# Kernel optimization log

Measured on AMD Instinct MI355X. Metric: run time of the kernel, lower is better.

## Reference

```python
import jax, jax.numpy as jnp
import numpy as np

N_NODES = 50000
N_EDGES = 300000
D = 256
N_RELS = 500


def setup_inputs() -> dict:
    key = jax.random.key(0)
    ks = jax.random.split(key, 12)
    s = 1.0 / np.sqrt(D)  # keep activations O(1) through the dense transforms
    return {
        "h": jax.random.normal(ks[0], (N_NODES, D), dtype=jnp.float32),
        "prev_h": jax.random.normal(ks[1], (N_NODES, D), dtype=jnp.float32),
        "emb_rel": jax.random.normal(ks[2], (N_RELS, D), dtype=jnp.float32),
        "norm": jax.random.uniform(ks[3], (N_NODES, 1), dtype=jnp.float32),
        "weight_neighbor": jax.random.normal(ks[4], (D, D), dtype=jnp.float32) * s,
        "loop_weight": jax.random.normal(ks[5], (D, D), dtype=jnp.float32) * s,
        "evolve_loop_weight": jax.random.normal(ks[6], (D, D), dtype=jnp.float32) * s,
        "skip_connect_weight": jax.random.normal(ks[7], (D, D), dtype=jnp.float32) * s,
        "skip_connect_bias": jnp.zeros((D,), dtype=jnp.float32),
        "src": jax.random.randint(ks[8], (N_EDGES,), 0, N_NODES),
        "dst": jax.random.randint(ks[9], (N_EDGES,), 0, N_NODES),
        "etype": jax.random.randint(ks[10], (N_EDGES,), 0, N_RELS),
    }


def reference(h, prev_h, emb_rel, norm, weight_neighbor, loop_weight,
              evolve_loop_weight, skip_connect_weight, skip_connect_bias,
              src, dst, etype):
    n_nodes = h.shape[0]
    # msg_func: per-edge gather of src features + relation embedding, dense transform
    msg = (h[src] + emb_rel[etype]) @ weight_neighbor          # [E, D]
    # fn.sum: segment-sum messages into destination nodes
    agg = jax.ops.segment_sum(msg, dst, num_segments=n_nodes)  # [N, D]
    # apply_func: multiply by per-node norm
    agg = agg * norm
    # self-loop: loop_weight where in_degree > 0, evolve_loop_weight otherwise
    in_deg = jax.ops.segment_sum(jnp.ones_like(dst), dst, num_segments=n_nodes)
    has_in = (in_deg > 0)[:, None]
    loop_message = jnp.where(has_in, h @ loop_weight, h @ evolve_loop_weight)
    # skip connection gate
    skip_weight = jax.nn.sigmoid(prev_h @ skip_connect_weight + skip_connect_bias)
    node_repr = skip_weight * (agg + loop_message) + (1.0 - skip_weight) * prev_h
    return jax.nn.relu(node_repr)
```

## Files before the change

### kernel.cpp

```cpp
#include <hip/hip_runtime.h>
#include <cstdint>
#include <cstddef>

#define N_NODES 50000
#define N_EDGES 300000
#define DIM     256
#define KTOT    768
#define N_RELS  500

#define SCAN_BLK  256
#define SCAN_NBLK ((N_NODES + SCAN_BLK - 1) / SCAN_BLK)

typedef unsigned short u16;
typedef __attribute__((ext_vector_type(8))) short short8v;
typedef __attribute__((ext_vector_type(4))) float float4v;

static __device__ __forceinline__ u16 f2bf(float f) {
    union { float f; unsigned u; } v; v.f = f;
    unsigned u = v.u;
    unsigned r = u + 0x7FFFu + ((u >> 16) & 1u);
    return (u16)(r >> 16);
}
static __device__ __forceinline__ float bf2f(u16 b) {
    union { unsigned u; float f; } v; v.u = ((unsigned)b) << 16; return v.f;
}

static __device__ __forceinline__ void gld16(const void* g, u16* l) {
    __builtin_amdgcn_global_load_lds(
        (const __attribute__((address_space(1))) unsigned int*)g,
        (__attribute__((address_space(3))) unsigned int*)l,
        16, 0, 0);
}

__global__ void conv_kernel(const float* __restrict__ h, const float* __restrict__ emb,
                            u16* __restrict__ Xcat, u16* __restrict__ embb) {
    int i = blockIdx.x * blockDim.x + threadIdx.x;
    int e0 = i * 8;
    if (e0 >= (N_NODES + N_RELS) * DIM) return;
    const float* src; u16* dst;
    if (e0 < N_NODES * DIM) {
        int n = e0 >> 8, c = e0 & 255;
        src = h + e0;
        dst = Xcat + (size_t)n * 512 + 256 + c;
    } else {
        int off = e0 - N_NODES * DIM;
        src = emb + off; dst = embb + off;
    }
    float4 a = *(const float4*)(src);
    float4 b = *(const float4*)(src + 4);
    u16 o[8] = { f2bf(a.x), f2bf(a.y), f2bf(a.z), f2bf(a.w),
                 f2bf(b.x), f2bf(b.y), f2bf(b.z), f2bf(b.w) };
    *(uint4*)dst = *(const uint4*)o;
}

__global__ void wt_kernel(const float* __restrict__ Wn, const float* __restrict__ Wl,
                          const float* __restrict__ Wsc, u16* __restrict__ Wt) {
    int k = blockIdx.x;
    int d = threadIdx.x;
    const float* W = (k < 256) ? Wn : ((k < 512) ? Wl : Wsc);
    int kk = k & 255;
    Wt[(size_t)d * KTOT + k] = f2bf(W[kk * DIM + d]);
}

__global__ void hist_kernel(const int* __restrict__ dstv, int* __restrict__ deg) {
    int e = blockIdx.x * 256 + threadIdx.x;
    if (e < N_EDGES) atomicAdd(&deg[dstv[e]], 1);
}

__global__ void scanA_kernel(const int* __restrict__ deg, int* __restrict__ excl_local,
                             int* __restrict__ block_sum) {
    __shared__ int sdata[SCAN_BLK];
    int t = threadIdx.x, i = blockIdx.x * SCAN_BLK + t;
    int v = (i < N_NODES) ? deg[i] : 0;
    sdata[t] = v;
    __syncthreads();
    for (int off = 1; off < SCAN_BLK; off <<= 1) {
        int u = (t >= off) ? sdata[t - off] : 0;
        __syncthreads();
        sdata[t] += u;
        __syncthreads();
    }
    if (i < N_NODES) excl_local[i] = sdata[t] - v;
    if (t == SCAN_BLK - 1) block_sum[blockIdx.x] = sdata[t];
}

__global__ void scanB_kernel(const int* __restrict__ block_sum, int* __restrict__ block_base,
                             int* __restrict__ offsets) {
    __shared__ int sdata[SCAN_NBLK];
    int t = threadIdx.x;
    int v = (t < SCAN_NBLK) ? block_sum[t] : 0;
    if (t < SCAN_NBLK) sdata[t] = v;
    __syncthreads();
    for (int off = 1; off < SCAN_NBLK; off <<= 1) {
        int u = (t >= off && t < SCAN_NBLK) ? sdata[t - off] : 0;
        __syncthreads();
        if (t < SCAN_NBLK) sdata[t] += u;
        __syncthreads();
    }
    if (t < SCAN_NBLK) block_base[t] = sdata[t] - v;
    if (t == SCAN_NBLK - 1) offsets[N_NODES] = sdata[t];
}

__global__ void scanC_kernel(const int* __restrict__ excl_local, const int* __restrict__ block_base,
                             int* __restrict__ offsets, int* __restrict__ cursor) {
    int i = blockIdx.x * SCAN_BLK + threadIdx.x;
    if (i < N_NODES) {
        int e = block_base[blockIdx.x] + excl_local[i];
        offsets[i] = e; cursor[i] = e;
    }
}

__global__ void scatter_kernel(const int* __restrict__ src, const int* __restrict__ dstv,
                               const int* __restrict__ et, int* __restrict__ cursor,
                               unsigned* __restrict__ esee) {
    int e = blockIdx.x * 256 + threadIdx.x;
    if (e >= N_EDGES) return;
    int d = dstv[e];
    int pos = atomicAdd(&cursor[d], 1);
    esee[pos] = (unsigned)src[e] * N_RELS + (unsigned)et[e];
}

__global__ void agg_kernel(u16* __restrict__ Xcat, const u16* __restrict__ embb,
                           const float* __restrict__ norm, const int* __restrict__ offsets,
                           const unsigned* __restrict__ esee,
                           int* __restrict__ wl_count, int* __restrict__ wl) {
    int wave = (blockIdx.x * 256 + threadIdx.x) >> 6;
    int lane = threadIdx.x & 63;
    if (wave >= N_NODES) return;
    int n = wave;
    int s0 = offsets[n], s1 = offsets[n + 1];
    int c4 = lane * 4;
    float4 acc = make_float4(0.f, 0.f, 0.f, 0.f);
    int e = s0;
    for (; e + 1 < s1; e += 2) {
        unsigned v0 = esee[e], v1 = esee[e + 1];
        unsigned sa = v0 / N_RELS, ta = v0 - sa * N_RELS;
        unsigned sb = v1 / N_RELS, tb = v1 - sb * N_RELS;
        ushort4 ha = *(const ushort4*)(Xcat + (size_t)sa * 512 + 256 + c4);
        ushort4 ea = *(const ushort4*)(embb + (size_t)ta * DIM + c4);
        ushort4 hb = *(const ushort4*)(Xcat + (size_t)sb * 512 + 256 + c4);
        ushort4 eb = *(const ushort4*)(embb + (size_t)tb * DIM + c4);
        acc.x += bf2f(ha.x) + bf2f(ea.x) + bf2f(hb.x) + bf2f(eb.x);
        acc.y += bf2f(ha.y) + bf2f(ea.y) + bf2f(hb.y) + bf2f(eb.y);
        acc.z += bf2f(ha.z) + bf2f(ea.z) + bf2f(hb.z) + bf2f(eb.z);
        acc.w += bf2f(ha.w) + bf2f(ea.w) + bf2f(hb.w) + bf2f(eb.w);
    }
    if (e < s1) {
        unsigned v = esee[e];
        unsigned s = v / N_RELS;
        unsigned t = v - s * N_RELS;
        ushort4 hv = *(const ushort4*)(Xcat + (size_t)s * 512 + 256 + c4);
        ushort4 ev = *(const ushort4*)(embb + (size_t)t * DIM + c4);
        acc.x += bf2f(hv.x) + bf2f(ev.x);
        acc.y += bf2f(hv.y) + bf2f(ev.y);
        acc.z += bf2f(hv.z) + bf2f(ev.z);
        acc.w += bf2f(hv.w) + bf2f(ev.w);
    }
    float nr = norm[n];
    u16 o[4] = { f2bf(acc.x * nr), f2bf(acc.y * nr), f2bf(acc.z * nr), f2bf(acc.w * nr) };
    *(ushort4*)(Xcat + (size_t)n * 512 + c4) = *(const ushort4*)o;
    if (lane == 0 && s1 == s0) { int idx = atomicAdd(wl_count, 1); wl[idx] = n; }
}

__launch_bounds__(256, 2)
__global__ void gemm_kernel(const u16* __restrict__ Xcat, const u16* __restrict__ Wt,
                            const float* __restrict__ prev_h, const float* __restrict__ bias,
                            float* __restrict__ out) {
    __shared__ __align__(16) u16 lds[40960];
    int tid  = threadIdx.x;
    int wave = tid >> 6, lane = tid & 63, q = lane >> 4, m16 = lane & 15;
    int wn = wave * 64;
    int m0 = blockIdx.x * 64;
    int lr = lane >> 3, lc8 = lane & 7;
    int scol = (lc8 ^ lr) << 3;

    int ar0 = wave * 16 + lr, ar1 = ar0 + 8;
    int ga0 = (m0 + ar0 < N_NODES) ? (m0 + ar0) : (N_NODES - 1);
    int ga1 = (m0 + ar1 < N_NODES) ? (m0 + ar1) : (N_NODES - 1);
    const u16*   sA0 = Xcat   + (size_t)ga0 * 512 + scol;
    const u16*   sA1 = Xcat   + (size_t)ga1 * 512 + scol;
    const float* pP0 = prev_h + (size_t)ga0 * 256 + scol;
    const float* pP1 = prev_h + (size_t)ga1 * 256 + scol;
    const u16*   sB  = Wt + (size_t)(wave * 64 + lr) * KTOT + scol;
    int ldsA_w = wave * 16 * 64;
    int ldsB_w = 8192 + wave * 64 * 64;

    float4v acc1[4][4], acc2[4][4];
#pragma unroll
    for (int i = 0; i < 4; i++)
#pragma unroll
        for (int j = 0; j < 4; j++) { acc1[i][j] = (float4v)0.f; acc2[i][j] = (float4v)0.f; }

#pragma unroll
    for (int j = 0; j < 8; j++)
        gld16(sB + (size_t)j * 8 * KTOT, &lds[ldsB_w + j * 512]);
    gld16(sA0, &lds[ldsA_w]);
    gld16(sA1, &lds[ldsA_w + 512]);
    __syncthreads();

    int sw = (m16 & 7) << 3;

#pragma unroll
    for (int kt = 0; kt < 12; kt++) {
        int buf = kt & 1, nbuf = buf ^ 1;
        float pf0[8], pf1[8];
        if (kt < 11) {
            int kn = kt + 1;
#pragma unroll
            for (int j = 0; j < 8; j++)
                gld16(sB + (size_t)j * 8 * KTOT + kn * 64,
                      &lds[ldsB_w + nbuf * 16384 + j * 512]);
            if (kn < 8) {
                gld16(sA0 + kn * 64, &lds[ldsA_w + nbuf * 4096]);
                gld16(sA1 + kn * 64, &lds[ldsA_w + nbuf * 4096 + 512]);
            } else {
                const float* p0 = pP0 + (kn - 8) * 64;
                const float* p1 = pP1 + (kn - 8) * 64;
                float4 x0 = *(const float4*)p0, y0 = *(const float4*)(p0 + 4);
                float4 x1 = *(const float4*)p1, y1 = *(const float4*)(p1 + 4);
                pf0[0] = x0.x; pf0[1] = x0.y; pf0[2] = x0.z; pf0[3] = x0.w;
                pf0[4] = y0.x; pf0[5] = y0.y; pf0[6] = y0.z; pf0[7] = y0.w;
                pf1[0] = x1.x; pf1[1] = x1.y; pf1[2] = x1.z; pf1[3] = x1.w;
                pf1[4] = y1.x; pf1[5] = y1.y; pf1[6] = y1.z; pf1[7] = y1.w;
            }
        }
#pragma unroll
        for (int kk = 0; kk < 2; kk++) {
            int ck = (kk * 32 + q * 8) ^ sw;
            short8v af[4], bfr[4];
#pragma unroll
            for (int mi = 0; mi < 4; mi++)
                af[mi] = *(const short8v*)(&lds[buf * 4096 + (mi * 16 + m16) * 64 + ck]);
#pragma unroll
            for (int ni = 0; ni < 4; ni++)
                bfr[ni] = *(const short8v*)(&lds[8192 + buf * 16384 + (wn + ni * 16 + m16) * 64 + ck]);
            if (kt < 8) {
#pragma unroll
                for (int mi = 0; mi < 4; mi++)
#pragma unroll
                    for (int ni = 0; ni < 4; ni++)
                        acc1[mi][ni] = __builtin_amdgcn_mfma_f32_16x16x32_bf16(
                            af[mi], bfr[ni], acc1[mi][ni], 0, 0, 0);
            } else {
#pragma unroll
                for (int mi = 0; mi < 4; mi++)
#pragma unroll
                    for (int ni = 0; ni < 4; ni++)
                        acc2[mi][ni] = __builtin_amdgcn_mfma_f32_16x16x32_bf16(
                            af[mi], bfr[ni], acc2[mi][ni], 0, 0, 0);
            }
        }
        if (kt < 11 && kt + 1 >= 8) {
            u16 o0[8] = { f2bf(pf0[0]), f2bf(pf0[1]), f2bf(pf0[2]), f2bf(pf0[3]),
                          f2bf(pf0[4]), f2bf(pf0[5]), f2bf(pf0[6]), f2bf(pf0[7]) };
            u16 o1[8] = { f2bf(pf1[0]), f2bf(pf1[1]), f2bf(pf1[2]), f2bf(pf1[3]),
                          f2bf(pf1[4]), f2bf(pf1[5]), f2bf(pf1[6]), f2bf(pf1[7]) };
            *(uint4*)(&lds[nbuf * 4096 + ar0 * 64 + lc8 * 8]) = *(const uint4*)o0;
            *(uint4*)(&lds[nbuf * 4096 + ar1 * 64 + lc8 * 8]) = *(const uint4*)o1;
        }
        __syncthreads();
    }

#pragma unroll
    for (int mi = 0; mi < 4; mi++) {
#pragma unroll
        for (int ni = 0; ni < 4; ni++) {
            int d = wn + ni * 16 + m16;
            float b = bias[d];
#pragma unroll
            for (int r = 0; r < 4; r++) {
                int node = m0 + mi * 16 + q * 4 + r;
                if (node < N_NODES) {
                    float S  = acc2[mi][ni][r] + b;
                    float sg = 1.f / (1.f + __expf(-S));
                    float ph = prev_h[(size_t)node * DIM + d];
                    float v  = sg * acc1[mi][ni][r] + (1.f - sg) * ph;
                    out[(size_t)node * DIM + d] = fmaxf(v, 0.f);
                }
            }
        }
    }
}

__global__ void fixup_kernel(const float* __restrict__ h, const float* __restrict__ prev_h,
                             const float* __restrict__ We, const float* __restrict__ Wsc,
                             const float* __restrict__ bias, const int* __restrict__ wl_count,
                             const int* __restrict__ wl, float* __restrict__ out) {
    __shared__ float ph[DIM], hh[DIM];
    int d = threadIdx.x;
    int cnt = *wl_count;
    for (int i = blockIdx.x; i < cnt; i += gridDim.x) {
        int n = wl[i];
        ph[d] = prev_h[(size_t)n * DIM + d];
        hh[d] = h[(size_t)n * DIM + d];
        __syncthreads();
        float s = 0.f, l = 0.f;
        for (int k = 0; k < DIM; k++) {
            s += ph[k] * Wsc[k * DIM + d];
            l += hh[k] * We[k * DIM + d];
        }
        float sg = 1.f / (1.f + __expf(-(s + bias[d])));
        float v = sg * l + (1.f - sg) * ph[d];
        out[(size_t)n * DIM + d] = fmaxf(v, 0.f);
        __syncthreads();
    }
}

extern "C" void kernel_launch(void* const* d_in, const int* in_sizes, int n_in,
                              void* d_out, int out_size, void* d_ws, size_t ws_size,
                              hipStream_t stream) {
    const float* h      = (const float*)d_in[0];
    const float* prev_h = (const float*)d_in[1];
    const float* emb    = (const float*)d_in[2];
    const float* norm   = (const float*)d_in[3];
    const float* Wn     = (const float*)d_in[4];
    const float* Wl     = (const float*)d_in[5];
    const float* We     = (const float*)d_in[6];
    const float* Wsc    = (const float*)d_in[7];
    const float* bias   = (const float*)d_in[8];
    const int*   src    = (const int*)d_in[9];
    const int*   dstv   = (const int*)d_in[10];
    const int*   et     = (const int*)d_in[11];
    float* out = (float*)d_out;

    char* ws = (char*)d_ws;
    size_t off = 0;
    auto alloc = [&](size_t bytes) -> char* {
        char* p = ws + off; off += (bytes + 255) & ~(size_t)255; return p;
    };
    u16* Xcat    = (u16*)alloc((size_t)N_NODES * 512 * 2);
    u16* embb    = (u16*)alloc((size_t)N_RELS * DIM * 2);
    u16* Wt      = (u16*)alloc((size_t)DIM * KTOT * 2);
    int* deg     = (int*)alloc((size_t)N_NODES * 4);
    int* wlcnt   = (int*)alloc(16);
    int* wl      = (int*)alloc((size_t)N_NODES * 4);
    int* offsets = (int*)alloc((size_t)(N_NODES + 1) * 4);
    int* cursor  = (int*)alloc((size_t)N_NODES * 4);
    unsigned* esee = (unsigned*)alloc((size_t)N_EDGES * 4);
    int* excl    = (int*)alloc((size_t)N_NODES * 4);
    int* bsum    = (int*)alloc((size_t)SCAN_NBLK * 4);
    int* bbase   = (int*)alloc((size_t)SCAN_NBLK * 4);

    hipMemsetAsync(deg, 0, (size_t)N_NODES * 4, stream);
    hipMemsetAsync(wlcnt, 0, 4, stream);

    conv_kernel<<<((N_NODES + N_RELS) * DIM / 8 + 255) / 256, 256, 0, stream>>>(h, emb, Xcat, embb);
    wt_kernel<<<KTOT, 256, 0, stream>>>(Wn, Wl, Wsc, Wt);
    hist_kernel<<<(N_EDGES + 255) / 256, 256, 0, stream>>>(dstv, deg);
    scanA_kernel<<<SCAN_NBLK, SCAN_BLK, 0, stream>>>(deg, excl, bsum);
    scanB_kernel<<<1, SCAN_BLK, 0, stream>>>(bsum, bbase, offsets);
    scanC_kernel<<<SCAN_NBLK, SCAN_BLK, 0, stream>>>(excl, bbase, offsets, cursor);
    scatter_kernel<<<(N_EDGES + 255) / 256, 256, 0, stream>>>(src, dstv, et, cursor, esee);
    agg_kernel<<<(N_NODES + 3) / 4, 256, 0, stream>>>(Xcat, embb, norm, offsets, esee, wlcnt, wl);
    gemm_kernel<<<(N_NODES + 63) / 64, 256, 0, stream>>>(Xcat, Wt, prev_h, bias, out);
    fixup_kernel<<<256, 256, 0, stream>>>(h, prev_h, We, Wsc, bias, wlcnt, wl, out);
}
```

Measured before the change: 317.7 us.

## Fuse prep kernels, pre-convert prev_h to bf16, pipeline GEMM loads two stages deep

Merges the conversion, weight-transpose and histogram kernels into one launch and adds a bf16 copy of prev_h to a widened Xcat row (768 columns). The GEMM then loads all 12 K-tiles uniformly through global_load_lds, issuing loads two tiles ahead with explicit vmcnt waits and raw barriers instead of converting prev_h in registers. The aggregation loop is unrolled by four edges. The extra prev_h conversion pass adds memory traffic up front and the hand-written waitcnt logic is fragile.

```diff
diff --git a/kernel.cpp b/kernel.cpp
--- a/kernel.cpp
+++ b/kernel.cpp
@@ -7,9 +7,14 @@
 #define DIM     256
 #define KTOT    768
 #define N_RELS  500
+#define XW      768
 
 #define SCAN_BLK  256
 #define SCAN_NBLK ((N_NODES + SCAN_BLK - 1) / SCAN_BLK)
+
+#define CONV_ELEMS ((2 * N_NODES + N_RELS) * DIM)
+#define CONV_BLKS  ((CONV_ELEMS / 8 + 255) / 256)
+#define HIST_BLKS  ((N_EDGES + 255) / 256)
 
 typedef unsigned short u16;
 typedef __attribute__((ext_vector_type(8))) short short8v;
@@ -32,39 +37,43 @@
         16, 0, 0);
 }
 
-__global__ void conv_kernel(const float* __restrict__ h, const float* __restrict__ emb,
-                            u16* __restrict__ Xcat, u16* __restrict__ embb) {
-    int i = blockIdx.x * blockDim.x + threadIdx.x;
-    int e0 = i * 8;
-    if (e0 >= (N_NODES + N_RELS) * DIM) return;
-    const float* src; u16* dst;
-    if (e0 < N_NODES * DIM) {
-        int n = e0 >> 8, c = e0 & 255;
-        src = h + e0;
-        dst = Xcat + (size_t)n * 512 + 256 + c;
+__global__ void prep_kernel(const float* __restrict__ h, const float* __restrict__ prev_h,
+                            const float* __restrict__ emb,
+                            const float* __restrict__ Wn, const float* __restrict__ Wl,
+                            const float* __restrict__ Wsc, const int* __restrict__ dstv,
+                            u16* __restrict__ Xcat, u16* __restrict__ embb,
+                            u16* __restrict__ Wt, int* __restrict__ deg) {
+    int b = blockIdx.x;
+    if (b < CONV_BLKS) {
+        int i = b * 256 + threadIdx.x;
+        int e0 = i * 8;
+        if (e0 >= CONV_ELEMS) return;
+        const float* s; u16* d;
+        if (e0 < N_NODES * DIM) {
+            int n = e0 >> 8, c = e0 & 255;
+            s = h + e0; d = Xcat + (size_t)n * XW + 256 + c;
+        } else if (e0 < 2 * N_NODES * DIM) {
+            int o = e0 - N_NODES * DIM;
+            int n = o >> 8, c = o & 255;
+            s = prev_h + o; d = Xcat + (size_t)n * XW + 512 + c;
+        } else {
+            int o = e0 - 2 * N_NODES * DIM;
+            s = emb + o; d = embb + o;
+        }
+        float4 a = *(const float4*)(s);
+        float4 c2 = *(const float4*)(s + 4);
+        u16 o8[8] = { f2bf(a.x), f2bf(a.y), f2bf(a.z), f2bf(a.w),
+                      f2bf(c2.x), f2bf(c2.y), f2bf(c2.z), f2bf(c2.w) };
+        *(uint4*)d = *(const uint4*)o8;
+    } else if (b < CONV_BLKS + KTOT) {
+        int k = b - CONV_BLKS;
+        int dd = threadIdx.x;
+        const float* W = (k < 256) ? Wn : ((k < 512) ? Wl : Wsc);
+        Wt[(size_t)dd * KTOT + k] = f2bf(W[(k & 255) * DIM + dd]);
     } else {
-        int off = e0 - N_NODES * DIM;
-        src = emb + off; dst = embb + off;
-    }
-    float4 a = *(const float4*)(src);
-    float4 b = *(const float4*)(src + 4);
-    u16 o[8] = { f2bf(a.x), f2bf(a.y), f2bf(a.z), f2bf(a.w),
-                 f2bf(b.x), f2bf(b.y), f2bf(b.z), f2bf(b.w) };
-    *(uint4*)dst = *(const uint4*)o;
-}
-
-__global__ void wt_kernel(const float* __restrict__ Wn, const float* __restrict__ Wl,
-                          const float* __restrict__ Wsc, u16* __restrict__ Wt) {
-    int k = blockIdx.x;
-    int d = threadIdx.x;
-    const float* W = (k < 256) ? Wn : ((k < 512) ? Wl : Wsc);
-    int kk = k & 255;
-    Wt[(size_t)d * KTOT + k] = f2bf(W[kk * DIM + d]);
-}
-
-__global__ void hist_kernel(const int* __restrict__ dstv, int* __restrict__ deg) {
-    int e = blockIdx.x * 256 + threadIdx.x;
-    if (e < N_EDGES) atomicAdd(&deg[dstv[e]], 1);
+        int e = (b - CONV_BLKS - KTOT) * 256 + threadIdx.x;
+        if (e < N_EDGES) atomicAdd(&deg[dstv[e]], 1);
+    }
 }
 
 __global__ void scanA_kernel(const int* __restrict__ deg, int* __restrict__ excl_local,
@@ -132,24 +141,34 @@
     int c4 = lane * 4;
     float4 acc = make_float4(0.f, 0.f, 0.f, 0.f);
     int e = s0;
-    for (; e + 1 < s1; e += 2) {
-        unsigned v0 = esee[e], v1 = esee[e + 1];
+    for (; e + 3 < s1; e += 4) {
+        unsigned v0 = esee[e], v1 = esee[e + 1], v2 = esee[e + 2], v3 = esee[e + 3];
         unsigned sa = v0 / N_RELS, ta = v0 - sa * N_RELS;
         unsigned sb = v1 / N_RELS, tb = v1 - sb * N_RELS;
-        ushort4 ha = *(const ushort4*)(Xcat + (size_t)sa * 512 + 256 + c4);
+        unsigned sc = v2 / N_RELS, tc = v2 - sc * N_RELS;
+        unsigned sd = v3 / N_RELS, td = v3 - sd * N_RELS;
+        ushort4 ha = *(const ushort4*)(Xcat + (size_t)sa * XW + 256 + c4);
         ushort4 ea = *(const ushort4*)(embb + (size_t)ta * DIM + c4);
-        ushort4 hb = *(const ushort4*)(Xcat + (size_t)sb * 512 + 256 + c4);
+        ushort4 hb = *(const ushort4*)(Xcat + (size_t)sb * XW + 256 + c4);
         ushort4 eb = *(const ushort4*)(embb + (size_t)tb * DIM + c4);
-        acc.x += bf2f(ha.x) + bf2f(ea.x) + bf2f(hb.x) + bf2f(eb.x);
-        acc.y += bf2f(ha.y) + bf2f(ea.y) + bf2f(hb.y) + bf2f(eb.y);
-        acc.z += bf2f(ha.z) + bf2f(ea.z) + bf2f(hb.z) + bf2f(eb.z);
-        acc.w += bf2f(ha.w) + bf2f(ea.w) + bf2f(hb.w) + bf2f(eb.w);
-    }
-    if (e < s1) {
+        ushort4 hc = *(const ushort4*)(Xcat + (size_t)sc * XW + 256 + c4);
+        ushort4 ec = *(const ushort4*)(embb + (size_t)tc * DIM + c4);
+        ushort4 hd = *(const ushort4*)(Xcat + (size_t)sd * XW + 256 + c4);
+        ushort4 ed = *(const ushort4*)(embb + (size_t)td * DIM + c4);
+        acc.x += (bf2f(ha.x) + bf2f(ea.x)) + (bf2f(hb.x) + bf2f(eb.x))
+               + (bf2f(hc.x) + bf2f(ec.x)) + (bf2f(hd.x) + bf2f(ed.x));
+        acc.y += (bf2f(ha.y) + bf2f(ea.y)) + (bf2f(hb.y) + bf2f(eb.y))
+               + (bf2f(hc.y) + bf2f(ec.y)) + (bf2f(hd.y) + bf2f(ed.y));
+        acc.z += (bf2f(ha.z) + bf2f(ea.z)) + (bf2f(hb.z) + bf2f(eb.z))
+               + (bf2f(hc.z) + bf2f(ec.z)) + (bf2f(hd.z) + bf2f(ed.z));
+        acc.w += (bf2f(ha.w) + bf2f(ea.w)) + (bf2f(hb.w) + bf2f(eb.w))
+               + (bf2f(hc.w) + bf2f(ec.w)) + (bf2f(hd.w) + bf2f(ed.w));
+    }
+    for (; e < s1; e++) {
         unsigned v = esee[e];
         unsigned s = v / N_RELS;
         unsigned t = v - s * N_RELS;
-        ushort4 hv = *(const ushort4*)(Xcat + (size_t)s * 512 + 256 + c4);
+        ushort4 hv = *(const ushort4*)(Xcat + (size_t)s * XW + 256 + c4);
         ushort4 ev = *(const ushort4*)(embb + (size_t)t * DIM + c4);
         acc.x += bf2f(hv.x) + bf2f(ev.x);
         acc.y += bf2f(hv.y) + bf2f(ev.y);
@@ -158,7 +177,7 @@
     }
     float nr = norm[n];
     u16 o[4] = { f2bf(acc.x * nr), f2bf(acc.y * nr), f2bf(acc.z * nr), f2bf(acc.w * nr) };
-    *(ushort4*)(Xcat + (size_t)n * 512 + c4) = *(const ushort4*)o;
+    *(ushort4*)(Xcat + (size_t)n * XW + c4) = *(const ushort4*)o;
     if (lane == 0 && s1 == s0) { int idx = atomicAdd(wl_count, 1); wl[idx] = n; }
 }
 
@@ -177,11 +196,9 @@
     int ar0 = wave * 16 + lr, ar1 = ar0 + 8;
     int ga0 = (m0 + ar0 < N_NODES) ? (m0 + ar0) : (N_NODES - 1);
     int ga1 = (m0 + ar1 < N_NODES) ? (m0 + ar1) : (N_NODES - 1);
-    const u16*   sA0 = Xcat   + (size_t)ga0 * 512 + scol;
-    const u16*   sA1 = Xcat   + (size_t)ga1 * 512 + scol;
-    const float* pP0 = prev_h + (size_t)ga0 * 256 + scol;
-    const float* pP1 = prev_h + (size_t)ga1 * 256 + scol;
-    const u16*   sB  = Wt + (size_t)(wave * 64 + lr) * KTOT + scol;
+    const u16* sA0 = Xcat + (size_t)ga0 * XW + scol;
+    const u16* sA1 = Xcat + (size_t)ga1 * XW + scol;
+    const u16* sB  = Wt + (size_t)(wave * 64 + lr) * KTOT + scol;
     int ldsA_w = wave * 16 * 64;
     int ldsB_w = 8192 + wave * 64 * 64;
 
@@ -191,39 +208,28 @@
 #pragma unroll
         for (int j = 0; j < 4; j++) { acc1[i][j] = (float4v)0.f; acc2[i][j] = (float4v)0.f; }
 
-#pragma unroll
-    for (int j = 0; j < 8; j++)
-        gld16(sB + (size_t)j * 8 * KTOT, &lds[ldsB_w + j * 512]);
-    gld16(sA0, &lds[ldsA_w]);
-    gld16(sA1, &lds[ldsA_w + 512]);
-    __syncthreads();
+    auto stage = [&](int kt, int buf) {
+#pragma unroll
+        for (int j = 0; j < 8; j++)
+            gld16(sB + (size_t)j * 8 * KTOT + kt * 64, &lds[ldsB_w + buf * 16384 + j * 512]);
+        gld16(sA0 + kt * 64, &lds[ldsA_w + buf * 4096]);
+        gld16(sA1 + kt * 64, &lds[ldsA_w + buf * 4096 + 512]);
+    };
+
+    stage(0, 0);
+    stage(1, 1);
 
     int sw = (m16 & 7) << 3;
 
 #pragma unroll
     for (int kt = 0; kt < 12; kt++) {
-        int buf = kt & 1, nbuf = buf ^ 1;
-        float pf0[8], pf1[8];
-        if (kt < 11) {
-            int kn = kt + 1;
-#pragma unroll
-            for (int j = 0; j < 8; j++)
-                gld16(sB + (size_t)j * 8 * KTOT + kn * 64,
-                      &lds[ldsB_w + nbuf * 16384 + j * 512]);
-            if (kn < 8) {
-                gld16(sA0 + kn * 64, &lds[ldsA_w + nbuf * 4096]);
-                gld16(sA1 + kn * 64, &lds[ldsA_w + nbuf * 4096 + 512]);
-            } else {
-                const float* p0 = pP0 + (kn - 8) * 64;
-                const float* p1 = pP1 + (kn - 8) * 64;
-                float4 x0 = *(const float4*)p0, y0 = *(const float4*)(p0 + 4);
-                float4 x1 = *(const float4*)p1, y1 = *(const float4*)(p1 + 4);
-                pf0[0] = x0.x; pf0[1] = x0.y; pf0[2] = x0.z; pf0[3] = x0.w;
-                pf0[4] = y0.x; pf0[5] = y0.y; pf0[6] = y0.z; pf0[7] = y0.w;
-                pf1[0] = x1.x; pf1[1] = x1.y; pf1[2] = x1.z; pf1[3] = x1.w;
-                pf1[4] = y1.x; pf1[5] = y1.y; pf1[6] = y1.z; pf1[7] = y1.w;
-            }
-        }
+        int buf = kt & 1;
+        if (kt < 11) asm volatile("s_waitcnt vmcnt(10)" ::: "memory");
+        else         asm volatile("s_waitcnt vmcnt(0)"  ::: "memory");
+        __builtin_amdgcn_sched_barrier(0);
+        __builtin_amdgcn_s_barrier();
+        __builtin_amdgcn_sched_barrier(0);
+
 #pragma unroll
         for (int kk = 0; kk < 2; kk++) {
             int ck = (kk * 32 + q * 8) ^ sw;
@@ -250,15 +256,11 @@
                             af[mi], bfr[ni], acc2[mi][ni], 0, 0, 0);
             }
         }
-        if (kt < 11 && kt + 1 >= 8) {
-            u16 o0[8] = { f2bf(pf0[0]), f2bf(pf0[1]), f2bf(pf0[2]), f2bf(pf0[3]),
-                          f2bf(pf0[4]), f2bf(pf0[5]), f2bf(pf0[6]), f2bf(pf0[7]) };
-            u16 o1[8] = { f2bf(pf1[0]), f2bf(pf1[1]), f2bf(pf1[2]), f2bf(pf1[3]),
-                          f2bf(pf1[4]), f2bf(pf1[5]), f2bf(pf1[6]), f2bf(pf1[7]) };
-            *(uint4*)(&lds[nbuf * 4096 + ar0 * 64 + lc8 * 8]) = *(const uint4*)o0;
-            *(uint4*)(&lds[nbuf * 4096 + ar1 * 64 + lc8 * 8]) = *(const uint4*)o1;
-        }
-        __syncthreads();
+
+        __builtin_amdgcn_sched_barrier(0);
+        __builtin_amdgcn_s_barrier();
+        __builtin_amdgcn_sched_barrier(0);
+        if (kt + 2 < 12) stage(kt + 2, buf);
     }
 
 #pragma unroll
@@ -328,7 +330,7 @@
     auto alloc = [&](size_t bytes) -> char* {
         char* p = ws + off; off += (bytes + 255) & ~(size_t)255; return p;
     };
-    u16* Xcat    = (u16*)alloc((size_t)N_NODES * 512 * 2);
+    u16* Xcat    = (u16*)alloc((size_t)N_NODES * XW * 2);
     u16* embb    = (u16*)alloc((size_t)N_RELS * DIM * 2);
     u16* Wt      = (u16*)alloc((size_t)DIM * KTOT * 2);
     int* deg     = (int*)alloc((size_t)N_NODES * 4);
@@ -344,9 +346,8 @@
     hipMemsetAsync(deg, 0, (size_t)N_NODES * 4, stream);
     hipMemsetAsync(wlcnt, 0, 4, stream);
 
-    conv_kernel<<<((N_NODES + N_RELS) * DIM / 8 + 255) / 256, 256, 0, stream>>>(h, emb, Xcat, embb);
-    wt_kernel<<<KTOT, 256, 0, stream>>>(Wn, Wl, Wsc, Wt);
-    hist_kernel<<<(N_EDGES + 255) / 256, 256, 0, stream>>>(dstv, deg);
+    prep_kernel<<<CONV_BLKS + KTOT + HIST_BLKS, 256, 0, stream>>>(
+        h, prev_h, emb, Wn, Wl, Wsc, dstv, Xcat, embb, Wt, deg);
     scanA_kernel<<<SCAN_NBLK, SCAN_BLK, 0, stream>>>(deg, excl, bsum);
     scanB_kernel<<<1, SCAN_BLK, 0, stream>>>(bsum, bbase, offsets);
     scanC_kernel<<<SCAN_NBLK, SCAN_BLK, 0, stream>>>(excl, bbase, offsets, cursor);
```

Result: no change. 319.0 us (+0.4%).
